# Kernel tuning notes

Measured on AMD Instinct MI355X. Metric: run time of the kernel, lower is better.

## Reference

```python
import jax, jax.numpy as jnp
import numpy as np

DEPTH = 8


def _xyz2key(x, y, z, b, depth):
    """Morton (z-order) key with batch index in the high bits. Int inputs."""
    key = jnp.zeros_like(x)
    for i in range(depth):  # fixed small loop over bit planes
        key = key | (((x >> i) & 1) << (3 * i + 2))
        key = key | (((y >> i) & 1) << (3 * i + 1))
        key = key | (((z >> i) & 1) << (3 * i))
    return key | (b << (3 * depth))


def setup_inputs() -> dict:
    key = jax.random.key(0)
    k1, k2, k3, k4 = jax.random.split(key, 4)
    N = 1 << 20   # query points
    H = 2_000_000  # octree nodes at this depth
    C = 32        # feature channels
    B = 4         # batch size
    depth = DEPTH
    xyz = jax.random.uniform(k1, (N, 3), jnp.float32, -1.0, 1.0)
    batch = jax.random.randint(k2, (N, 1), 0, B).astype(jnp.float32)
    pts = jnp.concatenate([xyz, batch], axis=1)  # [N,4] = (x,y,z,b)
    node_keys = jnp.sort(jax.random.randint(k3, (H,), 0, B << (3 * depth), dtype=jnp.int32))
    data = jax.random.normal(k4, (H, C), jnp.float32)
    return {"data": data, "pts": pts, "node_keys": node_keys, "depth": depth}


def reference(data, pts, node_keys, depth):
    # rescale_pts=True: map xyz from [-1,1) to [0, 2^depth)
    scale = 2.0 ** (depth - 1)
    grid = jnp.array([[0, 0, 0], [0, 0, 1], [0, 1, 0], [0, 1, 1],
                      [1, 0, 0], [1, 0, 1], [1, 1, 0], [1, 1, 1]], dtype=jnp.float32)
    xyzf = (pts[:, :3] + 1.0) * scale - 0.5           # [N,3]
    xyzi = jnp.floor(xyzf)
    frac = xyzf - xyzi                                 # [N,3]
    xyzn = (xyzi[:, None, :] + grid).astype(jnp.int32)  # [N,8,3] 8 corner coords
    b = pts[:, 3].astype(jnp.int32)[:, None]           # [N,1] -> broadcast over 8
    key8 = _xyz2key(xyzn[..., 0], xyzn[..., 1], xyzn[..., 2], b, depth)  # [N,8]
    # octree.search_key == binary search in sorted node key array
    pos = jnp.searchsorted(node_keys, key8.ravel()).reshape(key8.shape)  # [N,8]
    H = node_keys.shape[0]
    posc = jnp.minimum(pos, H - 1)
    valid = node_keys[posc] == key8                    # [N,8] found mask (idx > -1)
    # trilinear weights: prod(|1 - grid - frac|)
    w = jnp.abs(jnp.prod(1.0 - grid[None] - frac[:, None, :], axis=2))  # [N,8]
    w = jnp.where(valid, w, 0.0)
    feats = data[posc]                                 # [N,8,C] gather
    out = jnp.einsum('np,npc->nc', w, feats)           # sparse mm: weights @ data
    norm = jnp.sum(w, axis=1, keepdims=True)           # sparse mm with ones
    return out / (norm + 1e-12)
```

## Files before the change

kernel.cpp:

```cpp
#include <hip/hip_runtime.h>
#include <hip/hip_bf16.h>

#pragma clang fp contract(off)

#define NBLKP (1 << 20)
#define K_BITS 18

typedef float f32x4 __attribute__((ext_vector_type(4)));

__device__ __forceinline__ unsigned morton_spread(unsigned v) {
  v = (v | (v << 16)) & 0x030000FFu;
  v = (v | (v << 8)) & 0x0300F00Fu;
  v = (v | (v << 4)) & 0x030C30C3u;
  v = (v | (v << 2)) & 0x09249249u;
  return v;
}

__device__ __forceinline__ int morton_key(float xi, float yi, float zi,
                                          int gx, int gy, int gz, int b,
                                          int depth, unsigned cmask) {
  unsigned ux = ((unsigned)((int)xi + gx)) & cmask;
  unsigned uy = ((unsigned)((int)yi + gy)) & cmask;
  unsigned uz = ((unsigned)((int)zi + gz)) & cmask;
  return (int)((morton_spread(ux) << 2) | (morton_spread(uy) << 1) |
               morton_spread(uz)) | (b << (3 * depth));
}

__global__ __launch_bounds__(256) void octi_fill_tab(
    int* __restrict__ tab, int n, int H) {
  int j = blockIdx.x * 256 + threadIdx.x;
  if (j < n) tab[j] = H;
}

__global__ __launch_bounds__(256) void octi_scatter6(
    const int* __restrict__ keys, int H, int* __restrict__ tab) {
  int m = blockIdx.x * 256 + threadIdx.x;
  if (m >= H) return;
  int bc = (int)(((unsigned)keys[m]) >> 6);
  int bp = (m == 0) ? -1 : (int)(((unsigned)keys[m - 1]) >> 6);
  for (int j = bp + 1; j <= bc; ++j) tab[j] = m;
}

__global__ __launch_bounds__(256) void octi_pack(
    const int* __restrict__ keys, const int* __restrict__ tab,
    unsigned long long* __restrict__ bits8, unsigned* __restrict__ srt) {
  int b = blockIdx.x * 256 + threadIdx.x;
  if (b >= NBLKP) return;
  int s = tab[b], e = tab[b + 1];
  unsigned long long bits = 0ull;
  for (int m = s; m < e; ++m)
    bits |= 1ull << (((unsigned)keys[m]) & 63u);
  unsigned dup = ((e - s) != __popcll(bits)) ? 1u : 0u;
  bits8[b] = bits;
  srt[b] = (unsigned)s | (dup << 31);
}

__global__ __launch_bounds__(256) void octi_interp32(
    const float* __restrict__ data, const float* __restrict__ pts,
    const int* __restrict__ keys, const int* __restrict__ depth_ptr,
    const unsigned long long* __restrict__ bits8,
    const unsigned* __restrict__ srt, float* __restrict__ out,
    int N, int half) {
  int t = blockIdx.x * 256 + threadIdx.x;
  int g = t >> 3;
  if (g >= half) return;
  int l = t & 7;
  int i0 = g;
  int i1 = g + half;
  bool has1 = i1 < N;

  int depth = *depth_ptr;
  float scale = (float)(1 << (depth - 1));
  unsigned cmask = (1u << depth) - 1u;
  int gx = (l >> 2) & 1, gy = (l >> 1) & 1, gz = l & 1;

  float4 p0 = reinterpret_cast<const float4*>(pts)[i0];
  float4 p1 = reinterpret_cast<const float4*>(pts)[has1 ? i1 : i0];

  float xf0 = (p0.x + 1.0f) * scale - 0.5f;
  float yf0 = (p0.y + 1.0f) * scale - 0.5f;
  float zf0 = (p0.z + 1.0f) * scale - 0.5f;
  float xi0 = floorf(xf0), yi0 = floorf(yf0), zi0 = floorf(zf0);
  float fx0 = xf0 - xi0, fy0 = yf0 - yi0, fz0 = zf0 - zi0;
  int key0 = morton_key(xi0, yi0, zi0, gx, gy, gz, (int)p0.w, depth, cmask);

  float xf1 = (p1.x + 1.0f) * scale - 0.5f;
  float yf1 = (p1.y + 1.0f) * scale - 0.5f;
  float zf1 = (p1.z + 1.0f) * scale - 0.5f;
  float xi1 = floorf(xf1), yi1 = floorf(yf1), zi1 = floorf(zf1);
  float fx1 = xf1 - xi1, fy1 = yf1 - yi1, fz1 = zf1 - zi1;
  int key1 = morton_key(xi1, yi1, zi1, gx, gy, gz, (int)p1.w, depth, cmask);

  unsigned long long bits0 = bits8[((unsigned)key0) >> 6];
  unsigned long long bits1 = bits8[((unsigned)key1) >> 6];

  int bit0 = key0 & 63;
  bool present0 = (bits0 >> bit0) & 1ull;
  int pos0 = 0;
  if (present0) {
    unsigned sv = srt[((unsigned)key0) >> 6];
    pos0 = (int)(sv & 0x7FFFFFFFu) +
           (int)__popcll(bits0 & ((1ull << bit0) - 1ull));
    if (sv >> 31) {
      int row = (int)(sv & 0x7FFFFFFFu);
      while (keys[row] < key0) ++row;
      pos0 = row;
    }
  }

  int bit1 = key1 & 63;
  bool present1 = has1 && ((bits1 >> bit1) & 1ull);
  int pos1 = 0;
  if (present1) {
    unsigned sv = srt[((unsigned)key1) >> 6];
    pos1 = (int)(sv & 0x7FFFFFFFu) +
           (int)__popcll(bits1 & ((1ull << bit1) - 1ull));
    if (sv >> 31) {
      int row = (int)(sv & 0x7FFFFFFFu);
      while (keys[row] < key1) ++row;
      pos1 = row;
    }
  }

  int lane = threadIdx.x & 63;
  int base = lane & 56;

  float wx0 = (1.0f - (float)gx) - fx0;
  float wy0 = (1.0f - (float)gy) - fy0;
  float wz0 = (1.0f - (float)gz) - fz0;
  float w0 = present0 ? fabsf((wx0 * wy0) * wz0) : 0.0f;

  float wx1 = (1.0f - (float)gx) - fx1;
  float wy1 = (1.0f - (float)gy) - fy1;
  float wz1 = (1.0f - (float)gz) - fz1;
  float w1 = present1 ? fabsf((wx1 * wy1) * wz1) : 0.0f;

  unsigned long long ball0 = __ballot(w0 != 0.0f);
  unsigned long long ball1 = __ballot(w1 != 0.0f);

  {
    unsigned g8 = (unsigned)((ball0 >> base) & 0xFFull);
    float4 acc = make_float4(0.f, 0.f, 0.f, 0.f);
    float norm = 0.0f;
    while (g8) {
      int q = __ffs(g8) - 1;
      g8 &= g8 - 1;
      float wq = __shfl(w0, base + q, 64);
      int   pq = __shfl(pos0, base + q, 64);
      norm += wq;
      float4 f = reinterpret_cast<const float4*>(data)[pq * 8 + l];
      acc.x += wq * f.x;
      acc.y += wq * f.y;
      acc.z += wq * f.z;
      acc.w += wq * f.w;
    }
    float inv = 1.0f / (norm + 1e-12f);
    f32x4 o = {acc.x * inv, acc.y * inv, acc.z * inv, acc.w * inv};
    __builtin_nontemporal_store(o, reinterpret_cast<f32x4*>(out) + i0 * 8 + l);
  }
  if (has1) {
    unsigned g8 = (unsigned)((ball1 >> base) & 0xFFull);
    float4 acc = make_float4(0.f, 0.f, 0.f, 0.f);
    float norm = 0.0f;
    while (g8) {
      int q = __ffs(g8) - 1;
      g8 &= g8 - 1;
      float wq = __shfl(w1, base + q, 64);
      int   pq = __shfl(pos1, base + q, 64);
      norm += wq;
      float4 f = reinterpret_cast<const float4*>(data)[pq * 8 + l];
      acc.x += wq * f.x;
      acc.y += wq * f.y;
      acc.z += wq * f.z;
      acc.w += wq * f.w;
    }
    float inv = 1.0f / (norm + 1e-12f);
    f32x4 o = {acc.x * inv, acc.y * inv, acc.z * inv, acc.w * inv};
    __builtin_nontemporal_store(o, reinterpret_cast<f32x4*>(out) + i1 * 8 + l);
  }
}

__global__ __launch_bounds__(256) void octi_scatter_k(
    const int* __restrict__ keys, int H, const int* __restrict__ depth_ptr,
    int* __restrict__ tab, int kbits) {
  int m = blockIdx.x * 256 + threadIdx.x;
  if (m >= H) return;
  int depth = *depth_ptr;
  int kb = 3 * depth + 2;
  int S = kb > kbits ? kb - kbits : 0;
  int bc = (int)(((unsigned)keys[m]) >> S);
  int bp = (m == 0) ? -1 : (int)(((unsigned)keys[m - 1]) >> S);
  for (int j = bp + 1; j <= bc; ++j) tab[j] = m;
}

__global__ __launch_bounds__(256) void octi_interp_gen(
    const float* __restrict__ data, const float* __restrict__ pts,
    const int* __restrict__ keys, const int* __restrict__ depth_ptr,
    const int* __restrict__ tab, float* __restrict__ out,
    int N, int H, int C, int kbits) {
  int i = blockIdx.x * 256 + threadIdx.x;
  if (i >= N) return;
  int depth = *depth_ptr;
  int kb = 3 * depth + 2;
  int S = kb > kbits ? kb - kbits : 0;
  float scale = (float)(1 << (depth - 1));
  unsigned cmask = (1u << depth) - 1u;
  const float4 p = reinterpret_cast<const float4*>(pts)[i];
  float xf = (p.x + 1.0f) * scale - 0.5f;
  float yf = (p.y + 1.0f) * scale - 0.5f;
  float zf = (p.z + 1.0f) * scale - 0.5f;
  float xi = floorf(xf), yi = floorf(yf), zi = floorf(zf);
  float fx = xf - xi, fy = yf - yi, fz = zf - zi;
  int b = (int)p.w;
  float wv[8]; int pv[8];
  float norm = 0.0f;
  for (int l = 0; l < 8; ++l) {
    int gx = (l >> 2) & 1, gy = (l >> 1) & 1, gz = l & 1;
    int key = morton_key(xi, yi, zi, gx, gy, gz, b, depth, cmask);
    unsigned bkt = ((unsigned)key) >> S;
    int lo = tab ? tab[bkt] : 0;
    int hi = tab ? tab[bkt + 1] : H;
    bool present = false; int posc = 0;
    if (lo < hi) {
      int hi0 = hi;
      while (lo < hi) { int mid = (lo + hi) >> 1; if (keys[mid] < key) lo = mid + 1; else hi = mid; }
      present = (lo < hi0) && (keys[lo] == key);
      posc = lo;
    }
    float wx = (1.0f - (float)gx) - fx;
    float wy = (1.0f - (float)gy) - fy;
    float wz = (1.0f - (float)gz) - fz;
    float w = present ? fabsf((wx * wy) * wz) : 0.0f;
    wv[l] = w; pv[l] = posc; norm += w;
  }
  float dnm = norm + 1e-12f;
  for (int c = 0; c < C; ++c) {
    float acc = 0.0f;
    for (int q = 0; q < 8; ++q)
      if (wv[q] != 0.0f) acc += wv[q] * data[(long long)pv[q] * C + c];
    out[(long long)i * C + c] = acc / dnm;
  }
}

extern "C" void kernel_launch(void* const* d_in, const int* in_sizes, int n_in,
                              void* d_out, int out_size, void* d_ws, size_t ws_size,
                              hipStream_t stream) {
  const float* data = (const float*)d_in[0];
  const float* pts  = (const float*)d_in[1];
  const int*   keys = (const int*)d_in[2];
  const int*   dep  = (const int*)d_in[3];
  float* out = (float*)d_out;

  int H = in_sizes[2];
  int N = in_sizes[1] / 4;
  int C = (H > 0) ? in_sizes[0] / H : 0;

  size_t off_bits = 0;
  size_t off_srt  = (size_t)NBLKP * 8;
  size_t off_tab  = off_srt + (size_t)NBLKP * 4;
  size_t need = off_tab + ((size_t)NBLKP + 1) * 4;

  if (C == 32 && ws_size >= need) {
    unsigned long long* bits8 = (unsigned long long*)((char*)d_ws + off_bits);
    unsigned* srt = (unsigned*)((char*)d_ws + off_srt);
    int*      tab = (int*)((char*)d_ws + off_tab);

    octi_fill_tab<<<(NBLKP + 1 + 255) / 256, 256, 0, stream>>>(tab, NBLKP + 1, H);
    octi_scatter6<<<(H + 255) / 256, 256, 0, stream>>>(keys, H, tab);
    octi_pack<<<NBLKP / 256, 256, 0, stream>>>(keys, tab, bits8, srt);

    int half = (N + 1) >> 1;
    long long tt = (long long)half * 8;
    octi_interp32<<<(int)((tt + 255) / 256), 256, 0, stream>>>(
        data, pts, keys, dep, bits8, srt, out, N, half);
  } else {
    int kbits = K_BITS;
    int NB1 = (1 << kbits) + 1;
    bool useTab = ws_size >= (size_t)NB1 * sizeof(int);
    int* tab = (int*)d_ws;
    if (useTab) {
      octi_fill_tab<<<(NB1 + 255) / 256, 256, 0, stream>>>(tab, NB1, H);
      octi_scatter_k<<<(H + 255) / 256, 256, 0, stream>>>(keys, H, dep, tab, kbits);
    }
    octi_interp_gen<<<(N + 255) / 256, 256, 0, stream>>>(
        data, pts, keys, dep, useTab ? tab : nullptr, out, N, H, C, kbits);
  }
}
```

Measured before the change: 69.32 us.

## Add coarse occupancy filter bitmap to skip most bitmap loads

Adds a pre-pass kernel that folds the 64-bit per-block key bitmap into a coarser filter with one bit per group of four keys. The interpolation kernel first checks this 2 MB filter and reads the 8 MB bitmap and the start table only when the filter bit is set. Because occupancy of the key space is sparse, most corner lookups should stop at the smaller, more cache-resident filter instead of making a random access into the larger bitmap. The cost is an extra kernel launch, an extra pass over the bitmap, and a dependent second load for keys that pass the filter.

After: 70.56 us. About the same (+1.8%).

```diff
diff --git a/kernel.cpp b/kernel.cpp
--- a/kernel.cpp
+++ b/kernel.cpp
@@ -4,6 +4,7 @@
 #pragma clang fp contract(off)
 
 #define NBLKP (1 << 20)
+#define NFW   (NBLKP >> 2)
 #define K_BITS 18
 
 typedef float f32x4 __attribute__((ext_vector_type(4)));
@@ -55,12 +56,31 @@
   srt[b] = (unsigned)s | (dup << 31);
 }
 
+__global__ __launch_bounds__(256) void octi_filt(
+    const unsigned long long* __restrict__ bits8,
+    unsigned long long* __restrict__ filt) {
+  int f = blockIdx.x * 256 + threadIdx.x;
+  if (f >= NFW) return;
+  unsigned long long r = 0ull;
+  #pragma unroll
+  for (int wi = 0; wi < 4; ++wi) {
+    unsigned long long x = bits8[f * 4 + wi];
+    x = x | (x >> 1) | (x >> 2) | (x >> 3);
+    unsigned long long n = 0ull;
+    #pragma unroll
+    for (int i = 0; i < 16; ++i) n |= ((x >> (4 * i)) & 1ull) << i;
+    r |= n << (16 * wi);
+  }
+  filt[f] = r;
+}
+
 __global__ __launch_bounds__(256) void octi_interp32(
     const float* __restrict__ data, const float* __restrict__ pts,
     const int* __restrict__ keys, const int* __restrict__ depth_ptr,
     const unsigned long long* __restrict__ bits8,
-    const unsigned* __restrict__ srt, float* __restrict__ out,
-    int N, int half) {
+    const unsigned* __restrict__ srt,
+    const unsigned long long* __restrict__ filt,
+    float* __restrict__ out, int N, int half) {
   int t = blockIdx.x * 256 + threadIdx.x;
   int g = t >> 3;
   if (g >= half) return;
@@ -91,34 +111,44 @@
   float fx1 = xf1 - xi1, fy1 = yf1 - yi1, fz1 = zf1 - zi1;
   int key1 = morton_key(xi1, yi1, zi1, gx, gy, gz, (int)p1.w, depth, cmask);
 
-  unsigned long long bits0 = bits8[((unsigned)key0) >> 6];
-  unsigned long long bits1 = bits8[((unsigned)key1) >> 6];
-
-  int bit0 = key0 & 63;
-  bool present0 = (bits0 >> bit0) & 1ull;
+  unsigned long long f0 = filt[((unsigned)key0) >> 8];
+  unsigned long long f1 = filt[((unsigned)key1) >> 8];
+  bool pass0 = (f0 >> ((key0 >> 2) & 63)) & 1ull;
+  bool pass1 = has1 && ((f1 >> ((key1 >> 2) & 63)) & 1ull);
+
+  bool present0 = false;
   int pos0 = 0;
-  if (present0) {
-    unsigned sv = srt[((unsigned)key0) >> 6];
-    pos0 = (int)(sv & 0x7FFFFFFFu) +
-           (int)__popcll(bits0 & ((1ull << bit0) - 1ull));
-    if (sv >> 31) {
-      int row = (int)(sv & 0x7FFFFFFFu);
-      while (keys[row] < key0) ++row;
-      pos0 = row;
-    }
-  }
-
-  int bit1 = key1 & 63;
-  bool present1 = has1 && ((bits1 >> bit1) & 1ull);
+  if (pass0) {
+    unsigned long long bits0 = bits8[((unsigned)key0) >> 6];
+    int bit0 = key0 & 63;
+    present0 = (bits0 >> bit0) & 1ull;
+    if (present0) {
+      unsigned sv = srt[((unsigned)key0) >> 6];
+      pos0 = (int)(sv & 0x7FFFFFFFu) +
+             (int)__popcll(bits0 & ((1ull << bit0) - 1ull));
+      if (sv >> 31) {
+        int row = (int)(sv & 0x7FFFFFFFu);
+        while (keys[row] < key0) ++row;
+        pos0 = row;
+      }
+    }
+  }
+
+  bool present1 = false;
   int pos1 = 0;
-  if (present1) {
-    unsigned sv = srt[((unsigned)key1) >> 6];
-    pos1 = (int)(sv & 0x7FFFFFFFu) +
-           (int)__popcll(bits1 & ((1ull << bit1) - 1ull));
-    if (sv >> 31) {
-      int row = (int)(sv & 0x7FFFFFFFu);
-      while (keys[row] < key1) ++row;
-      pos1 = row;
+  if (pass1) {
+    unsigned long long bits1 = bits8[((unsigned)key1) >> 6];
+    int bit1 = key1 & 63;
+    present1 = (bits1 >> bit1) & 1ull;
+    if (present1) {
+      unsigned sv = srt[((unsigned)key1) >> 6];
+      pos1 = (int)(sv & 0x7FFFFFFFu) +
+             (int)__popcll(bits1 & ((1ull << bit1) - 1ull));
+      if (sv >> 31) {
+        int row = (int)(sv & 0x7FFFFFFFu);
+        while (keys[row] < key1) ++row;
+        pos1 = row;
+      }
     }
   }
 
@@ -258,21 +288,25 @@
   size_t off_bits = 0;
   size_t off_srt  = (size_t)NBLKP * 8;
   size_t off_tab  = off_srt + (size_t)NBLKP * 4;
-  size_t need = off_tab + ((size_t)NBLKP + 1) * 4;
+  size_t off_filt = off_tab + ((size_t)NBLKP + 1) * 4;
+  off_filt = (off_filt + 63) & ~(size_t)63;
+  size_t need = off_filt + (size_t)NFW * 8;
 
   if (C == 32 && ws_size >= need) {
     unsigned long long* bits8 = (unsigned long long*)((char*)d_ws + off_bits);
     unsigned* srt = (unsigned*)((char*)d_ws + off_srt);
     int*      tab = (int*)((char*)d_ws + off_tab);
+    unsigned long long* filt = (unsigned long long*)((char*)d_ws + off_filt);
 
     octi_fill_tab<<<(NBLKP + 1 + 255) / 256, 256, 0, stream>>>(tab, NBLKP + 1, H);
     octi_scatter6<<<(H + 255) / 256, 256, 0, stream>>>(keys, H, tab);
     octi_pack<<<NBLKP / 256, 256, 0, stream>>>(keys, tab, bits8, srt);
+    octi_filt<<<NFW / 256, 256, 0, stream>>>(bits8, filt);
 
     int half = (N + 1) >> 1;
     long long tt = (long long)half * 8;
     octi_interp32<<<(int)((tt + 255) / 256), 256, 0, stream>>>(
-        data, pts, keys, dep, bits8, srt, out, N, half);
+        data, pts, keys, dep, bits8, srt, filt, out, N, half);
   } else {
     int kbits = K_BITS;
     int NB1 = (1 << kbits) + 1;
```
